# Kernel tuning notes

Measured on AMD Instinct MI355X. Metric: run time of the kernel, lower is better.

## Reference

```python
import jax, jax.numpy as jnp
import numpy as np

NUM_EMBEDDINGS = 1024
EMBEDDING_DIM = 64
COMMITMENT_COST = 0.25


def setup_inputs() -> dict:
    key = jax.random.key(0)
    k1, k2 = jax.random.split(key)
    inputs = jax.random.normal(k1, (64, 32, 32, EMBEDDING_DIM), dtype=jnp.float32)
    # torch init is uniform(-1/K, 1/K); scale accordingly
    weight = jax.random.uniform(
        k2, (NUM_EMBEDDINGS, EMBEDDING_DIM), dtype=jnp.float32,
        minval=-1.0 / NUM_EMBEDDINGS, maxval=1.0 / NUM_EMBEDDINGS)
    return {"inputs": inputs, "weight": weight}


def reference(inputs, weight):
    input_shape = inputs.shape
    flat = inputs.reshape(-1, EMBEDDING_DIM)               # [N, D]
    distances = (jnp.sum(flat ** 2, axis=1, keepdims=True)
                 + jnp.sum(weight ** 2, axis=1)
                 - 2.0 * flat @ weight.T)                   # [N, K]
    encoding_indices = jnp.argmin(distances, axis=1)        # [N]
    # gather codes (equivalent to one-hot @ weight, but as a direct gather)
    quantized = weight[encoding_indices].reshape(input_shape)

    e_latent_loss = jnp.mean((jax.lax.stop_gradient(quantized) - inputs) ** 2)
    q_latent_loss = jnp.mean((quantized - jax.lax.stop_gradient(inputs)) ** 2)
    loss = q_latent_loss + COMMITMENT_COST * e_latent_loss

    # straight-through estimator
    quantized_ste = inputs + jax.lax.stop_gradient(quantized - inputs)

    # perplexity (equivalent to mean over the one-hot encodings)
    n_tokens = flat.shape[0]
    counts = jax.ops.segment_sum(
        jnp.ones((n_tokens,), jnp.float32), encoding_indices,
        num_segments=NUM_EMBEDDINGS)
    avg_probs = counts / n_tokens
    perplexity = jnp.exp(-jnp.sum(avg_probs * jnp.log(avg_probs + 1e-10)))

    indices_for_transformer = encoding_indices.reshape(input_shape[0], -1)
    return (loss, quantized_ste, perplexity, indices_for_transformer)
```

## Files before the change

### kernel.cpp

```cpp
#include <hip/hip_runtime.h>
#include <cstdint>
#include <cstddef>

#define N_TOKENS 65536
#define DIM 64
#define K_CODES 1024
#define NTH 256
#define TPB 128
#define NCH 16

#define OFF_Q 1
#define OFF_PERP 4194305
#define OFF_IDX 4194306

#define MARGIN 1.5e-4f

#define WS_LOSS   0
#define WS_FCNT   8
#define WS_COUNTS 16
#define WS_WHI    4112
#define WS_WLO    135184
#define WS_S2     266256
#define WS_FLIST  270352

typedef __attribute__((ext_vector_type(8))) short  s16x8;
typedef __attribute__((ext_vector_type(4))) float  f32x4;

__device__ __forceinline__ float fmulr(float a, float b){ return __fmul_rn(a,b); }
__device__ __forceinline__ float faddr(float a, float b){ return __fadd_rn(a,b); }

__device__ __forceinline__ unsigned short f2bf(float f) {
    unsigned u = __float_as_uint(f);
    unsigned r = u + 0x7fffu + ((u >> 16) & 1u);
    return (unsigned short)(r >> 16);
}
__device__ __forceinline__ float bf2f(unsigned short h) {
    return __uint_as_float(((unsigned)h) << 16);
}

__device__ float sumsq64_np(const float* __restrict__ p) {
    float s[16];
    #pragma unroll
    for (int l = 0; l < 16; ++l) {
        float a0 = fmulr(p[l],      p[l]);
        float a1 = fmulr(p[l + 16], p[l + 16]);
        float a2 = fmulr(p[l + 32], p[l + 32]);
        float a3 = fmulr(p[l + 48], p[l + 48]);
        s[l] = faddr(faddr(a0, a1), faddr(a2, a3));
    }
    #pragma unroll
    for (int len = 8; len >= 1; len >>= 1)
        #pragma unroll
        for (int l = 0; l < len; ++l)
            s[l] = faddr(s[l], s[l + len]);
    return s[0];
}

__device__ __forceinline__ void async_copy16(const void* g, void* l) {
    __builtin_amdgcn_global_load_lds(
        (const __attribute__((address_space(1))) void*)g,
        (__attribute__((address_space(3))) void*)l, 16, 0, 0);
}

__global__ void vq_prep(const float* __restrict__ W, unsigned short* __restrict__ Whi,
                        unsigned short* __restrict__ Wlo, float* __restrict__ s2g,
                        int* __restrict__ counts, int* __restrict__ gfcount,
                        double* __restrict__ loss_acc) {
    int gid = blockIdx.x * NTH + threadIdx.x;
    for (int e = gid; e < K_CODES * DIM; e += 16384) {
        float x = W[e];
        unsigned short hi = f2bf(x);
        unsigned short lo = f2bf(__fsub_rn(x, bf2f(hi)));
        int j = e >> 6, k = e & 63;
        int pos = j * 64 + (((k >> 3) ^ (j & 7)) << 3) + (k & 7);
        Whi[pos] = hi; Wlo[pos] = lo;
    }
    if (gid < K_CODES) { s2g[gid] = sumsq64_np(W + gid * 64); counts[gid] = 0; }
    if (gid == 0) { *loss_acc = 0.0; *gfcount = 0; }
}

__global__ __launch_bounds__(NTH, 2)
void vq_main(const float* __restrict__ X, const float* __restrict__ W,
             const unsigned short* __restrict__ WhiG, const unsigned short* __restrict__ WloG,
             const float* __restrict__ s2g, float* __restrict__ out,
             double* __restrict__ loss_acc, int* __restrict__ counts,
             int* __restrict__ gfcount, unsigned short* __restrict__ gflist) {
    __shared__ __align__(16) unsigned short xs_hi[TPB * 64];
    __shared__ __align__(16) unsigned short xs_lo[TPB * 64];
    __shared__ __align__(16) unsigned short ws_hi[2][64 * 64];
    __shared__ __align__(16) unsigned short ws_lo[2][64 * 64];
    __shared__ __align__(16) float s2s[K_CODES];
    __shared__ int fidx[TPB];
    __shared__ int flist[TPB];
    __shared__ int fcount, gbaseS;
    __shared__ double lred[4];

    const int tid  = threadIdx.x;
    const int lane = tid & 63, wave = tid >> 6;
    const int quad = lane >> 4, lrow = lane & 15;
    const int t0   = blockIdx.x * TPB;

    if (tid == 0) fcount = 0;

    {
        const char* gh = (const char*)WhiG;
        const char* gl = (const char*)WloG;
        char* lh = (char*)&ws_hi[0][0] + wave * 1024;
        char* ll = (char*)&ws_lo[0][0] + wave * 1024;
        #pragma unroll
        for (int i = 0; i < 2; ++i) {
            async_copy16(gh + i * 4096 + tid * 16, lh + i * 4096);
            async_copy16(gl + i * 4096 + tid * 16, ll + i * 4096);
        }
    }
    *(f32x4*)&s2s[tid * 4] = *(const f32x4*)&s2g[tid * 4];
    #pragma unroll
    for (int i = 0; i < 4; ++i) {
        int g = tid + NTH * i;
        int t = g >> 3, kb = g & 7;
        const float* src = X + (size_t)(t0 + t) * DIM + kb * 8;
        float v[8];
        *(f32x4*)v       = *(const f32x4*)src;
        *(f32x4*)(v + 4) = *(const f32x4*)(src + 4);
        unsigned short h[8], l[8];
        #pragma unroll
        for (int k = 0; k < 8; ++k) {
            h[k] = f2bf(v[k]);
            l[k] = f2bf(__fsub_rn(v[k], bf2f(h[k])));
        }
        int base = t * 64 + ((kb ^ (t & 7)) << 3);
        *(s16x8*)&xs_hi[base] = *(s16x8*)h;
        *(s16x8*)&xs_lo[base] = *(s16x8*)l;
    }
    __syncthreads();

    s16x8 a_h0[2], a_h1[2], a_l0[2], a_l1[2];
    #pragma unroll
    for (int rt = 0; rt < 2; ++rt) {
        int tf = wave * 32 + rt * 16 + lrow;
        int sA = tf & 7;
        a_h0[rt] = *(const s16x8*)&xs_hi[tf * 64 + (((0 + quad) ^ sA) << 3)];
        a_h1[rt] = *(const s16x8*)&xs_hi[tf * 64 + (((4 + quad) ^ sA) << 3)];
        a_l0[rt] = *(const s16x8*)&xs_lo[tf * 64 + (((0 + quad) ^ sA) << 3)];
        a_l1[rt] = *(const s16x8*)&xs_lo[tf * 64 + (((4 + quad) ^ sA) << 3)];
    }

    float r1v[8], r2v[8]; int r1i[8];
    #pragma unroll
    for (int ri = 0; ri < 8; ++ri) { r1v[ri] = 3.4e38f; r2v[ri] = 3.4e38f; r1i[ri] = 0x7fffffff; }

    for (int ch = 0; ch < NCH; ++ch) {
        const int buf = ch & 1;
        if (ch < NCH - 1) {
            const char* gh = (const char*)WhiG + (ch + 1) * 8192;
            const char* gl = (const char*)WloG + (ch + 1) * 8192;
            char* lh = (char*)&ws_hi[buf ^ 1][0] + wave * 1024;
            char* ll = (char*)&ws_lo[buf ^ 1][0] + wave * 1024;
            #pragma unroll
            for (int i = 0; i < 2; ++i) {
                async_copy16(gh + i * 4096 + tid * 16, lh + i * 4096);
                async_copy16(gl + i * 4096 + tid * 16, ll + i * 4096);
            }
        }
        #pragma unroll
        for (int ct = 0; ct < 4; ++ct) {
            int lc = ct * 16 + lrow;
            int sB = lrow & 7;
            const unsigned short* bh = &ws_hi[buf][lc * 64];
            const unsigned short* bl = &ws_lo[buf][lc * 64];
            s16x8 b_h0 = *(const s16x8*)&bh[((0 + quad) ^ sB) << 3];
            s16x8 b_h1 = *(const s16x8*)&bh[((4 + quad) ^ sB) << 3];
            s16x8 b_l0 = *(const s16x8*)&bl[((0 + quad) ^ sB) << 3];
            s16x8 b_l1 = *(const s16x8*)&bl[((4 + quad) ^ sB) << 3];
            int jcode = ch * 64 + lc;
            float s2v = s2s[jcode];
            float ainit = fmulr(-0.5f, s2v);
            #pragma unroll
            for (int rt = 0; rt < 2; ++rt) {
                f32x4 acc = {ainit, ainit, ainit, ainit};
                acc = __builtin_amdgcn_mfma_f32_16x16x32_bf16(a_h0[rt], b_h0, acc, 0, 0, 0);
                acc = __builtin_amdgcn_mfma_f32_16x16x32_bf16(a_h1[rt], b_h1, acc, 0, 0, 0);
                acc = __builtin_amdgcn_mfma_f32_16x16x32_bf16(a_h0[rt], b_l0, acc, 0, 0, 0);
                acc = __builtin_amdgcn_mfma_f32_16x16x32_bf16(a_h1[rt], b_l1, acc, 0, 0, 0);
                acc = __builtin_amdgcn_mfma_f32_16x16x32_bf16(a_l0[rt], b_h0, acc, 0, 0, 0);
                acc = __builtin_amdgcn_mfma_f32_16x16x32_bf16(a_l1[rt], b_h1, acc, 0, 0, 0);
                #pragma unroll
                for (int r = 0; r < 4; ++r) {
                    float d = fmulr(-2.0f, acc[r]);
                    int ri = rt * 4 + r;
                    bool lt = d < r1v[ri];
                    float sec = lt ? r1v[ri] : d;
                    r2v[ri] = fminf(r2v[ri], sec);
                    r1v[ri] = lt ? d : r1v[ri];
                    r1i[ri] = lt ? jcode : r1i[ri];
                }
            }
        }
        __syncthreads();
    }

    #pragma unroll
    for (int m = 1; m <= 8; m <<= 1) {
        #pragma unroll
        for (int ri = 0; ri < 8; ++ri) {
            float o1v = __shfl_xor(r1v[ri], m, 64);
            int   o1i = __shfl_xor(r1i[ri], m, 64);
            float o2v = __shfl_xor(r2v[ri], m, 64);
            bool take = (o1v < r1v[ri]) || (o1v == r1v[ri] && o1i < r1i[ri]);
            float loser = take ? r1v[ri] : o1v;
            r2v[ri] = fminf(fminf(r2v[ri], o2v), loser);
            if (take) { r1v[ri] = o1v; r1i[ri] = o1i; }
        }
    }
    if (lrow == 0) {
        #pragma unroll
        for (int ri = 0; ri < 8; ++ri) {
            int rt = ri >> 2, r = ri & 3;
            int t = wave * 32 + rt * 16 + quad * 4 + r;
            bool fb = (r2v[ri] - r1v[ri]) < MARGIN;
            fidx[t] = fb ? (r1i[ri] | (int)0x80000000) : r1i[ri];
            if (fb) { int p = atomicAdd(&fcount, 1); flist[p] = t; }
        }
    }
    __syncthreads();

    double lsum = 0.0;
    #pragma unroll
    for (int i = 0; i < 8; ++i) {
        int e4 = tid + NTH * i;
        int t = e4 >> 4, d4 = (e4 & 15) * 4;
        int iv = fidx[t];
        if (iv >= 0) {
            f32x4 q = *(const f32x4*)&W[iv * 64 + d4];
            f32x4 x = *(const f32x4*)&X[(size_t)(t0 + t) * 64 + d4];
            *(f32x4*)&out[(size_t)OFF_Q + (size_t)(t0 + t) * 64 + d4] = q;
            #pragma unroll
            for (int c = 0; c < 4; ++c) {
                float df = __fsub_rn(q[c], x[c]);
                lsum += (double)fmulr(df, df);
            }
        }
    }
    #pragma unroll
    for (int off = 32; off >= 1; off >>= 1) lsum += __shfl_down(lsum, off, 64);
    if (lane == 0) lred[wave] = lsum;
    if (tid < TPB) {
        int iv = fidx[tid];
        if (iv >= 0) {
            atomicAdd(&counts[iv], 1);
            out[(size_t)OFF_IDX + t0 + tid] = (float)iv;
        }
    }
    if (tid == 0) gbaseS = atomicAdd(gfcount, fcount);
    __syncthreads();
    if (tid < fcount) gflist[gbaseS + tid] = (unsigned short)(t0 + flist[tid]);
    if (tid == 0) atomicAdd(loss_acc, lred[0] + lred[1] + lred[2] + lred[3]);
}

__global__ __launch_bounds__(NTH, 3)
void vq_fallback(const float* __restrict__ X, const float* __restrict__ W,
                 const float* __restrict__ s2g, const int* __restrict__ gfcount,
                 const unsigned short* __restrict__ gflist, float* __restrict__ out,
                 double* __restrict__ loss_acc, int* __restrict__ counts) {
    int count = *gfcount;
    int base = blockIdx.x * 64;
    if (base >= count) return;
    int nt = min(64, count - base);

    __shared__ __align__(16) float xsf[64 * 64];
    __shared__ __align__(16) float wsf[128 * 64];
    __shared__ float s1f[64];
    __shared__ int gidx[64];
    __shared__ double lredf[4];

    const int tid = threadIdx.x;
    const int lane = tid & 63, wave = tid >> 6;
    const int r = tid & 15, c = tid >> 4;

    #pragma unroll
    for (int i = 0; i < 4; ++i) {
        int idx = tid + NTH * i;
        int t = idx >> 4, kb = idx & 15;
        int tok = gflist[base + (t < nt ? t : 0)];
        f32x4 v = *(const f32x4*)(X + (size_t)tok * 64 + kb * 4);
        *(f32x4*)&xsf[t * 64 + ((kb ^ ((t >> 2) & 7)) << 2)] = v;
    }
    if (tid < nt) s1f[tid] = sumsq64_np(X + (size_t)gflist[base + tid] * 64);

    float runVal[4]; int runIdx[4];
    #pragma unroll
    for (int i = 0; i < 4; ++i) { runVal[i] = 3.4e38f; runIdx[i] = 0; }

    for (int ch = 0; ch < 8; ++ch) {
        __syncthreads();
        #pragma unroll
        for (int i = 0; i < 8; ++i) {
            int idx = tid + NTH * i;
            int jl = idx >> 4, kb = idx & 15;
            f32x4 v = *(const f32x4*)(W + (size_t)(ch * 128 + jl) * 64 + kb * 4);
            *(f32x4*)&wsf[jl * 64 + ((kb ^ ((jl >> 3) & 7)) << 2)] = v;
        }
        __syncthreads();

        float acc[4][8];
        #pragma unroll
        for (int i = 0; i < 4; ++i)
            #pragma unroll
            for (int m = 0; m < 8; ++m) acc[i][m] = 0.0f;

        #pragma unroll
        for (int kb = 0; kb < 16; ++kb) {
            f32x4 xv[4], wv[8];
            #pragma unroll
            for (int i = 0; i < 4; ++i)
                xv[i] = *(const f32x4*)&xsf[(4 * r + i) * 64 + ((kb ^ (r & 7)) << 2)];
            #pragma unroll
            for (int m = 0; m < 8; ++m)
                wv[m] = *(const f32x4*)&wsf[(8 * c + m) * 64 + ((kb ^ (c & 7)) << 2)];
            #pragma unroll
            for (int i = 0; i < 4; ++i)
                #pragma unroll
                for (int m = 0; m < 8; ++m) {
                    acc[i][m] = __builtin_fmaf(xv[i][0], wv[m][0], acc[i][m]);
                    acc[i][m] = __builtin_fmaf(xv[i][1], wv[m][1], acc[i][m]);
                    acc[i][m] = __builtin_fmaf(xv[i][2], wv[m][2], acc[i][m]);
                    acc[i][m] = __builtin_fmaf(xv[i][3], wv[m][3], acc[i][m]);
                }
        }
        #pragma unroll
        for (int i = 0; i < 4; ++i) {
            float s1v = s1f[4 * r + i];
            #pragma unroll
            for (int m = 0; m < 8; ++m) {
                int jl = 8 * c + m;
                float d = faddr(faddr(s1v, s2g[ch * 128 + jl]), fmulr(-2.0f, acc[i][m]));
                if (d < runVal[i]) { runVal[i] = d; runIdx[i] = ch * 128 + jl; }
            }
        }
    }

    __syncthreads();
    unsigned long long* red = (unsigned long long*)wsf;
    #pragma unroll
    for (int i = 0; i < 4; ++i) {
        unsigned long long pk =
            ((unsigned long long)__float_as_uint(runVal[i]) << 32) |
            (unsigned long long)(unsigned int)runIdx[i];
        red[(4 * r + i) * 16 + c] = pk;
    }
    __syncthreads();
    if (tid < 64) {
        unsigned long long best = red[tid * 16];
        #pragma unroll
        for (int cc = 1; cc < 16; ++cc) {
            unsigned long long v = red[tid * 16 + cc];
            best = (v < best) ? v : best;
        }
        int idx = (int)(best & 0xffffffffu);
        gidx[tid] = idx;
        if (tid < nt) {
            int tok = gflist[base + tid];
            out[(size_t)OFF_IDX + tok] = (float)idx;
            atomicAdd(&counts[idx], 1);
        }
    }
    __syncthreads();
    double lsum = 0.0;
    #pragma unroll
    for (int i = 0; i < 4; ++i) {
        int e4 = tid + NTH * i;
        int t = e4 >> 4, d4 = (e4 & 15) * 4;
        if (t < nt) {
            int tok = gflist[base + t];
            int idx = gidx[t];
            f32x4 q = *(const f32x4*)&W[idx * 64 + d4];
            f32x4 x = *(const f32x4*)&X[(size_t)tok * 64 + d4];
            *(f32x4*)&out[(size_t)OFF_Q + (size_t)tok * 64 + d4] = q;
            #pragma unroll
            for (int cc = 0; cc < 4; ++cc) {
                float df = __fsub_rn(q[cc], x[cc]);
                lsum += (double)fmulr(df, df);
            }
        }
    }
    #pragma unroll
    for (int off = 32; off >= 1; off >>= 1) lsum += __shfl_down(lsum, off, 64);
    if (lane == 0) lredf[wave] = lsum;
    __syncthreads();
    if (tid == 0) atomicAdd(loss_acc, lredf[0] + lredf[1] + lredf[2] + lredf[3]);
}

__global__ void vq_final(const int* __restrict__ counts,
                         const double* __restrict__ loss_acc,
                         float* __restrict__ out) {
    __shared__ double hred[4];
    int tid = threadIdx.x;
    double h = 0.0;
    for (int j = tid; j < K_CODES; j += 256) {
        double p = (double)counts[j] / 65536.0;
        h += p * log(p + 1e-10);
    }
    #pragma unroll
    for (int off = 32; off >= 1; off >>= 1) h += __shfl_down(h, off, 64);
    if ((tid & 63) == 0) hred[tid >> 6] = h;
    __syncthreads();
    if (tid == 0) {
        double H = hred[0] + hred[1] + hred[2] + hred[3];
        out[OFF_PERP] = (float)exp(-H);
        double ls = *loss_acc;
        float Lf = (float)(ls / 4194304.0);
        out[0] = faddr(Lf, fmulr(0.25f, Lf));
    }
}

extern "C" void kernel_launch(void* const* d_in, const int* in_sizes, int n_in,
                              void* d_out, int out_size, void* d_ws, size_t ws_size,
                              hipStream_t stream) {
    const float* X = (const float*)d_in[0];
    const float* W = (const float*)d_in[1];
    float* out = (float*)d_out;
    char* ws = (char*)d_ws;
    double* loss_acc = (double*)(ws + WS_LOSS);
    int* gfcount = (int*)(ws + WS_FCNT);
    int* counts = (int*)(ws + WS_COUNTS);
    unsigned short* Whi = (unsigned short*)(ws + WS_WHI);
    unsigned short* Wlo = (unsigned short*)(ws + WS_WLO);
    float* s2g = (float*)(ws + WS_S2);
    unsigned short* gflist = (unsigned short*)(ws + WS_FLIST);

    vq_prep<<<64, NTH, 0, stream>>>(W, Whi, Wlo, s2g, counts, gfcount, loss_acc);
    vq_main<<<N_TOKENS / TPB, NTH, 0, stream>>>(X, W, Whi, Wlo, s2g, out,
                                                loss_acc, counts, gfcount, gflist);
    vq_fallback<<<N_TOKENS / 64, NTH, 0, stream>>>(X, W, s2g, gfcount, gflist,
                                                   out, loss_acc, counts);
    vq_final<<<1, NTH, 0, stream>>>(counts, loss_acc, out);
}
```

Measured before the change: 171.4 us.

## Switch split-precision MFMA to scaled fp16, inline fallback and fuse final reduction

Replaces the bf16 hi/lo split with a scaled fp16 hi/lo split. fp16 keeps more mantissa bits, so the ambiguity margin can be tightened and fewer tokens need the exact fp32 fallback. Ambiguous tokens are now recomputed inside the main kernel, one wave per token, and the last block to finish (tracked with a ticket counter) computes perplexity and loss. This removes the separate fallback and final kernels. Tokens per block double to 256 with occupancy 1, which adds register pressure and reduces latency hiding. The in-block fallback reads W straight from global memory, serialising per wave.

```diff
diff --git a/kernel.cpp b/kernel.cpp
--- a/kernel.cpp
+++ b/kernel.cpp
@@ -6,36 +6,41 @@
 #define DIM 64
 #define K_CODES 1024
 #define NTH 256
-#define TPB 128
+#define TPB 256
 #define NCH 16
+#define NBLK (N_TOKENS / TPB)
 
 #define OFF_Q 1
 #define OFF_PERP 4194305
 #define OFF_IDX 4194306
 
-#define MARGIN 1.5e-4f
+#define MARGIN 2.5e-5f
+#define XSCALE 1024.0f
+#define WSCALE 65536.0f
+#define AINIT_SC -33554432.0f
+#define D_UNSC  -2.9802322387695312e-08f
 
 #define WS_LOSS   0
-#define WS_FCNT   8
+#define WS_TICKET 8
 #define WS_COUNTS 16
 #define WS_WHI    4112
 #define WS_WLO    135184
 #define WS_S2     266256
-#define WS_FLIST  270352
-
-typedef __attribute__((ext_vector_type(8))) short  s16x8;
-typedef __attribute__((ext_vector_type(4))) float  f32x4;
+
+typedef _Float16 f16x8 __attribute__((ext_vector_type(8)));
+typedef float    f32x4 __attribute__((ext_vector_type(4)));
 
 __device__ __forceinline__ float fmulr(float a, float b){ return __fmul_rn(a,b); }
 __device__ __forceinline__ float faddr(float a, float b){ return __fadd_rn(a,b); }
 
-__device__ __forceinline__ unsigned short f2bf(float f) {
+__device__ __forceinline__ unsigned keyf(float f) {
     unsigned u = __float_as_uint(f);
-    unsigned r = u + 0x7fffu + ((u >> 16) & 1u);
-    return (unsigned short)(r >> 16);
-}
-__device__ __forceinline__ float bf2f(unsigned short h) {
-    return __uint_as_float(((unsigned)h) << 16);
+    return u ^ ((u & 0x80000000u) ? 0xffffffffu : 0x80000000u);
+}
+
+__device__ __forceinline__ void split16(float v, _Float16& h, _Float16& l) {
+    h = (_Float16)v;
+    l = (_Float16)(v - (float)h);
 }
 
 __device__ float sumsq64_np(const float* __restrict__ p) {
@@ -62,37 +67,36 @@
         (__attribute__((address_space(3))) void*)l, 16, 0, 0);
 }
 
-__global__ void vq_prep(const float* __restrict__ W, unsigned short* __restrict__ Whi,
-                        unsigned short* __restrict__ Wlo, float* __restrict__ s2g,
-                        int* __restrict__ counts, int* __restrict__ gfcount,
+__global__ void vq_prep(const float* __restrict__ W, _Float16* __restrict__ Whi,
+                        _Float16* __restrict__ Wlo, float* __restrict__ s2g,
+                        int* __restrict__ counts, int* __restrict__ ticket,
                         double* __restrict__ loss_acc) {
     int gid = blockIdx.x * NTH + threadIdx.x;
     for (int e = gid; e < K_CODES * DIM; e += 16384) {
-        float x = W[e];
-        unsigned short hi = f2bf(x);
-        unsigned short lo = f2bf(__fsub_rn(x, bf2f(hi)));
+        float vs = W[e] * WSCALE;
+        _Float16 h, l; split16(vs, h, l);
         int j = e >> 6, k = e & 63;
         int pos = j * 64 + (((k >> 3) ^ (j & 7)) << 3) + (k & 7);
-        Whi[pos] = hi; Wlo[pos] = lo;
+        Whi[pos] = h; Wlo[pos] = l;
     }
     if (gid < K_CODES) { s2g[gid] = sumsq64_np(W + gid * 64); counts[gid] = 0; }
-    if (gid == 0) { *loss_acc = 0.0; *gfcount = 0; }
-}
-
-__global__ __launch_bounds__(NTH, 2)
+    if (gid == 0) { *loss_acc = 0.0; *ticket = 0; }
+}
+
+__global__ __launch_bounds__(NTH, 1)
 void vq_main(const float* __restrict__ X, const float* __restrict__ W,
-             const unsigned short* __restrict__ WhiG, const unsigned short* __restrict__ WloG,
+             const _Float16* __restrict__ WhiG, const _Float16* __restrict__ WloG,
              const float* __restrict__ s2g, float* __restrict__ out,
              double* __restrict__ loss_acc, int* __restrict__ counts,
-             int* __restrict__ gfcount, unsigned short* __restrict__ gflist) {
-    __shared__ __align__(16) unsigned short xs_hi[TPB * 64];
-    __shared__ __align__(16) unsigned short xs_lo[TPB * 64];
-    __shared__ __align__(16) unsigned short ws_hi[2][64 * 64];
-    __shared__ __align__(16) unsigned short ws_lo[2][64 * 64];
+             int* __restrict__ ticket) {
+    __shared__ __align__(16) _Float16 xs_hi[TPB * 64];
+    __shared__ __align__(16) _Float16 xs_lo[TPB * 64];
+    __shared__ __align__(16) _Float16 ws_hi[2][64 * 64];
+    __shared__ __align__(16) _Float16 ws_lo[2][64 * 64];
     __shared__ __align__(16) float s2s[K_CODES];
     __shared__ int fidx[TPB];
     __shared__ int flist[TPB];
-    __shared__ int fcount, gbaseS;
+    __shared__ int fcount, lastFlag;
     __shared__ double lred[4];
 
     const int tid  = threadIdx.x;
@@ -115,39 +119,36 @@
     }
     *(f32x4*)&s2s[tid * 4] = *(const f32x4*)&s2g[tid * 4];
     #pragma unroll
-    for (int i = 0; i < 4; ++i) {
+    for (int i = 0; i < 8; ++i) {
         int g = tid + NTH * i;
         int t = g >> 3, kb = g & 7;
         const float* src = X + (size_t)(t0 + t) * DIM + kb * 8;
         float v[8];
         *(f32x4*)v       = *(const f32x4*)src;
         *(f32x4*)(v + 4) = *(const f32x4*)(src + 4);
-        unsigned short h[8], l[8];
-        #pragma unroll
-        for (int k = 0; k < 8; ++k) {
-            h[k] = f2bf(v[k]);
-            l[k] = f2bf(__fsub_rn(v[k], bf2f(h[k])));
-        }
+        _Float16 h[8], l[8];
+        #pragma unroll
+        for (int k = 0; k < 8; ++k) split16(v[k] * XSCALE, h[k], l[k]);
         int base = t * 64 + ((kb ^ (t & 7)) << 3);
-        *(s16x8*)&xs_hi[base] = *(s16x8*)h;
-        *(s16x8*)&xs_lo[base] = *(s16x8*)l;
-    }
-    __syncthreads();
-
-    s16x8 a_h0[2], a_h1[2], a_l0[2], a_l1[2];
-    #pragma unroll
-    for (int rt = 0; rt < 2; ++rt) {
-        int tf = wave * 32 + rt * 16 + lrow;
+        *(f16x8*)&xs_hi[base] = *(f16x8*)h;
+        *(f16x8*)&xs_lo[base] = *(f16x8*)l;
+    }
+    __syncthreads();
+
+    f16x8 a_h0[4], a_h1[4], a_l0[4], a_l1[4];
+    #pragma unroll
+    for (int rt = 0; rt < 4; ++rt) {
+        int tf = wave * 64 + rt * 16 + lrow;
         int sA = tf & 7;
-        a_h0[rt] = *(const s16x8*)&xs_hi[tf * 64 + (((0 + quad) ^ sA) << 3)];
-        a_h1[rt] = *(const s16x8*)&xs_hi[tf * 64 + (((4 + quad) ^ sA) << 3)];
-        a_l0[rt] = *(const s16x8*)&xs_lo[tf * 64 + (((0 + quad) ^ sA) << 3)];
-        a_l1[rt] = *(const s16x8*)&xs_lo[tf * 64 + (((4 + quad) ^ sA) << 3)];
-    }
-
-    float r1v[8], r2v[8]; int r1i[8];
-    #pragma unroll
-    for (int ri = 0; ri < 8; ++ri) { r1v[ri] = 3.4e38f; r2v[ri] = 3.4e38f; r1i[ri] = 0x7fffffff; }
+        a_h0[rt] = *(const f16x8*)&xs_hi[tf * 64 + (((0 + quad) ^ sA) << 3)];
+        a_h1[rt] = *(const f16x8*)&xs_hi[tf * 64 + (((4 + quad) ^ sA) << 3)];
+        a_l0[rt] = *(const f16x8*)&xs_lo[tf * 64 + (((0 + quad) ^ sA) << 3)];
+        a_l1[rt] = *(const f16x8*)&xs_lo[tf * 64 + (((4 + quad) ^ sA) << 3)];
+    }
+
+    float r1v[16], r2v[16]; int r1i[16];
+    #pragma unroll
+    for (int ri = 0; ri < 16; ++ri) { r1v[ri] = 3.4e38f; r2v[ri] = 3.4e38f; r1i[ri] = 0x7fffffff; }
 
     for (int ch = 0; ch < NCH; ++ch) {
         const int buf = ch & 1;
@@ -166,27 +167,26 @@
         for (int ct = 0; ct < 4; ++ct) {
             int lc = ct * 16 + lrow;
             int sB = lrow & 7;
-            const unsigned short* bh = &ws_hi[buf][lc * 64];
-            const unsigned short* bl = &ws_lo[buf][lc * 64];
-            s16x8 b_h0 = *(const s16x8*)&bh[((0 + quad) ^ sB) << 3];
-            s16x8 b_h1 = *(const s16x8*)&bh[((4 + quad) ^ sB) << 3];
-            s16x8 b_l0 = *(const s16x8*)&bl[((0 + quad) ^ sB) << 3];
-            s16x8 b_l1 = *(const s16x8*)&bl[((4 + quad) ^ sB) << 3];
+            const _Float16* bh = &ws_hi[buf][lc * 64];
+            const _Float16* bl = &ws_lo[buf][lc * 64];
+            f16x8 b_h0 = *(const f16x8*)&bh[((0 + quad) ^ sB) << 3];
+            f16x8 b_h1 = *(const f16x8*)&bh[((4 + quad) ^ sB) << 3];
+            f16x8 b_l0 = *(const f16x8*)&bl[((0 + quad) ^ sB) << 3];
+            f16x8 b_l1 = *(const f16x8*)&bl[((4 + quad) ^ sB) << 3];
             int jcode = ch * 64 + lc;
-            float s2v = s2s[jcode];
-            float ainit = fmulr(-0.5f, s2v);
+            float ainit = fmulr(s2s[jcode], AINIT_SC);
             #pragma unroll
-            for (int rt = 0; rt < 2; ++rt) {
+            for (int rt = 0; rt < 4; ++rt) {
                 f32x4 acc = {ainit, ainit, ainit, ainit};
-                acc = __builtin_amdgcn_mfma_f32_16x16x32_bf16(a_h0[rt], b_h0, acc, 0, 0, 0);
-                acc = __builtin_amdgcn_mfma_f32_16x16x32_bf16(a_h1[rt], b_h1, acc, 0, 0, 0);
-                acc = __builtin_amdgcn_mfma_f32_16x16x32_bf16(a_h0[rt], b_l0, acc, 0, 0, 0);
-                acc = __builtin_amdgcn_mfma_f32_16x16x32_bf16(a_h1[rt], b_l1, acc, 0, 0, 0);
-                acc = __builtin_amdgcn_mfma_f32_16x16x32_bf16(a_l0[rt], b_h0, acc, 0, 0, 0);
-                acc = __builtin_amdgcn_mfma_f32_16x16x32_bf16(a_l1[rt], b_h1, acc, 0, 0, 0);
+                acc = __builtin_amdgcn_mfma_f32_16x16x32_f16(a_h0[rt], b_h0, acc, 0, 0, 0);
+                acc = __builtin_amdgcn_mfma_f32_16x16x32_f16(a_h1[rt], b_h1, acc, 0, 0, 0);
+                acc = __builtin_amdgcn_mfma_f32_16x16x32_f16(a_h0[rt], b_l0, acc, 0, 0, 0);
+                acc = __builtin_amdgcn_mfma_f32_16x16x32_f16(a_h1[rt], b_l1, acc, 0, 0, 0);
+                acc = __builtin_amdgcn_mfma_f32_16x16x32_f16(a_l0[rt], b_h0, acc, 0, 0, 0);
+                acc = __builtin_amdgcn_mfma_f32_16x16x32_f16(a_l1[rt], b_h1, acc, 0, 0, 0);
                 #pragma unroll
                 for (int r = 0; r < 4; ++r) {
-                    float d = fmulr(-2.0f, acc[r]);
+                    float d = fmulr(acc[r], D_UNSC);
                     int ri = rt * 4 + r;
                     bool lt = d < r1v[ri];
                     float sec = lt ? r1v[ri] : d;
@@ -202,7 +202,7 @@
     #pragma unroll
     for (int m = 1; m <= 8; m <<= 1) {
         #pragma unroll
-        for (int ri = 0; ri < 8; ++ri) {
+        for (int ri = 0; ri < 16; ++ri) {
             float o1v = __shfl_xor(r1v[ri], m, 64);
             int   o1i = __shfl_xor(r1i[ri], m, 64);
             float o2v = __shfl_xor(r2v[ri], m, 64);
@@ -214,9 +214,9 @@
     }
     if (lrow == 0) {
         #pragma unroll
-        for (int ri = 0; ri < 8; ++ri) {
+        for (int ri = 0; ri < 16; ++ri) {
             int rt = ri >> 2, r = ri & 3;
-            int t = wave * 32 + rt * 16 + quad * 4 + r;
+            int t = wave * 64 + rt * 16 + quad * 4 + r;
             bool fb = (r2v[ri] - r1v[ri]) < MARGIN;
             fidx[t] = fb ? (r1i[ri] | (int)0x80000000) : r1i[ri];
             if (fb) { int p = atomicAdd(&fcount, 1); flist[p] = t; }
@@ -226,7 +226,7 @@
 
     double lsum = 0.0;
     #pragma unroll
-    for (int i = 0; i < 8; ++i) {
+    for (int i = 0; i < 16; ++i) {
         int e4 = tid + NTH * i;
         int t = e4 >> 4, d4 = (e4 & 15) * 4;
         int iv = fidx[t];
@@ -251,165 +251,80 @@
             out[(size_t)OFF_IDX + t0 + tid] = (float)iv;
         }
     }
-    if (tid == 0) gbaseS = atomicAdd(gfcount, fcount);
-    __syncthreads();
-    if (tid < fcount) gflist[gbaseS + tid] = (unsigned short)(t0 + flist[tid]);
+    __syncthreads();
     if (tid == 0) atomicAdd(loss_acc, lred[0] + lred[1] + lred[2] + lred[3]);
-}
-
-__global__ __launch_bounds__(NTH, 3)
-void vq_fallback(const float* __restrict__ X, const float* __restrict__ W,
-                 const float* __restrict__ s2g, const int* __restrict__ gfcount,
-                 const unsigned short* __restrict__ gflist, float* __restrict__ out,
-                 double* __restrict__ loss_acc, int* __restrict__ counts) {
-    int count = *gfcount;
-    int base = blockIdx.x * 64;
-    if (base >= count) return;
-    int nt = min(64, count - base);
-
-    __shared__ __align__(16) float xsf[64 * 64];
-    __shared__ __align__(16) float wsf[128 * 64];
-    __shared__ float s1f[64];
-    __shared__ int gidx[64];
-    __shared__ double lredf[4];
-
-    const int tid = threadIdx.x;
-    const int lane = tid & 63, wave = tid >> 6;
-    const int r = tid & 15, c = tid >> 4;
-
-    #pragma unroll
-    for (int i = 0; i < 4; ++i) {
-        int idx = tid + NTH * i;
-        int t = idx >> 4, kb = idx & 15;
-        int tok = gflist[base + (t < nt ? t : 0)];
-        f32x4 v = *(const f32x4*)(X + (size_t)tok * 64 + kb * 4);
-        *(f32x4*)&xsf[t * 64 + ((kb ^ ((t >> 2) & 7)) << 2)] = v;
-    }
-    if (tid < nt) s1f[tid] = sumsq64_np(X + (size_t)gflist[base + tid] * 64);
-
-    float runVal[4]; int runIdx[4];
-    #pragma unroll
-    for (int i = 0; i < 4; ++i) { runVal[i] = 3.4e38f; runIdx[i] = 0; }
-
-    for (int ch = 0; ch < 8; ++ch) {
+
+    for (int fi = wave; fi < fcount; fi += 4) {
+        int t = flist[fi];
+        int gtok = t0 + t;
+        float s1v = sumsq64_np(X + (size_t)gtok * 64);
+        f32x4 xr[16];
+        #pragma unroll
+        for (int kb = 0; kb < 16; ++kb)
+            xr[kb] = *(const f32x4*)(X + (size_t)gtok * 64 + kb * 4);
+        unsigned long long best = ~0ULL;
+        #pragma unroll 1
+        for (int c16 = 0; c16 < 16; ++c16) {
+            int code = lane * 16 + c16;
+            const float* wr = W + code * 64;
+            float acc = 0.0f;
+            #pragma unroll
+            for (int kb = 0; kb < 16; ++kb) {
+                f32x4 wv = *(const f32x4*)(wr + kb * 4);
+                acc = __builtin_fmaf(xr[kb][0], wv[0], acc);
+                acc = __builtin_fmaf(xr[kb][1], wv[1], acc);
+                acc = __builtin_fmaf(xr[kb][2], wv[2], acc);
+                acc = __builtin_fmaf(xr[kb][3], wv[3], acc);
+            }
+            float d = faddr(faddr(s1v, s2s[code]), fmulr(-2.0f, acc));
+            unsigned long long pk = ((unsigned long long)keyf(d) << 32) | (unsigned)code;
+            best = pk < best ? pk : best;
+        }
+        #pragma unroll
+        for (int m = 32; m >= 1; m >>= 1) {
+            unsigned long long o = __shfl_xor(best, m, 64);
+            best = o < best ? o : best;
+        }
+        int idx = (int)(best & 0xffffffffu);
+        float q = W[idx * 64 + lane];
+        float x = X[(size_t)gtok * 64 + lane];
+        out[(size_t)OFF_Q + (size_t)gtok * 64 + lane] = q;
+        float df = __fsub_rn(q, x);
+        double ls = (double)fmulr(df, df);
+        #pragma unroll
+        for (int m = 32; m >= 1; m >>= 1) ls += __shfl_xor(ls, m, 64);
+        if (lane == 0) {
+            out[(size_t)OFF_IDX + gtok] = (float)idx;
+            atomicAdd(&counts[idx], 1);
+            atomicAdd(loss_acc, ls);
+        }
+    }
+
+    __syncthreads();
+    if (tid == 0) {
+        __threadfence();
+        int old = atomicAdd(ticket, 1);
+        lastFlag = (old == NBLK - 1) ? 1 : 0;
+    }
+    __syncthreads();
+    if (lastFlag) {
+        double h = 0.0;
+        for (int j = tid; j < K_CODES; j += NTH) {
+            int c = atomicAdd(&counts[j], 0);
+            double p = (double)c / 65536.0;
+            h += p * log(p + 1e-10);
+        }
+        #pragma unroll
+        for (int off = 32; off >= 1; off >>= 1) h += __shfl_down(h, off, 64);
+        if (lane == 0) lred[wave] = h;
         __syncthreads();
-        #pragma unroll
-        for (int i = 0; i < 8; ++i) {
-            int idx = tid + NTH * i;
-            int jl = idx >> 4, kb = idx & 15;
-            f32x4 v = *(const f32x4*)(W + (size_t)(ch * 128 + jl) * 64 + kb * 4);
-            *(f32x4*)&wsf[jl * 64 + ((kb ^ ((jl >> 3) & 7)) << 2)] = v;
-        }
-        __syncthreads();
-
-        float acc[4][8];
-        #pragma unroll
-        for (int i = 0; i < 4; ++i)
-            #pragma unroll
-            for (int m = 0; m < 8; ++m) acc[i][m] = 0.0f;
-
-        #pragma unroll
-        for (int kb = 0; kb < 16; ++kb) {
-            f32x4 xv[4], wv[8];
-            #pragma unroll
-            for (int i = 0; i < 4; ++i)
-                xv[i] = *(const f32x4*)&xsf[(4 * r + i) * 64 + ((kb ^ (r & 7)) << 2)];
-            #pragma unroll
-            for (int m = 0; m < 8; ++m)
-                wv[m] = *(const f32x4*)&wsf[(8 * c + m) * 64 + ((kb ^ (c & 7)) << 2)];
-            #pragma unroll
-            for (int i = 0; i < 4; ++i)
-                #pragma unroll
-                for (int m = 0; m < 8; ++m) {
-                    acc[i][m] = __builtin_fmaf(xv[i][0], wv[m][0], acc[i][m]);
-                    acc[i][m] = __builtin_fmaf(xv[i][1], wv[m][1], acc[i][m]);
-                    acc[i][m] = __builtin_fmaf(xv[i][2], wv[m][2], acc[i][m]);
-                    acc[i][m] = __builtin_fmaf(xv[i][3], wv[m][3], acc[i][m]);
-                }
-        }
-        #pragma unroll
-        for (int i = 0; i < 4; ++i) {
-            float s1v = s1f[4 * r + i];
-            #pragma unroll
-            for (int m = 0; m < 8; ++m) {
-                int jl = 8 * c + m;
-                float d = faddr(faddr(s1v, s2g[ch * 128 + jl]), fmulr(-2.0f, acc[i][m]));
-                if (d < runVal[i]) { runVal[i] = d; runIdx[i] = ch * 128 + jl; }
-            }
-        }
-    }
-
-    __syncthreads();
-    unsigned long long* red = (unsigned long long*)wsf;
-    #pragma unroll
-    for (int i = 0; i < 4; ++i) {
-        unsigned long long pk =
-            ((unsigned long long)__float_as_uint(runVal[i]) << 32) |
-            (unsigned long long)(unsigned int)runIdx[i];
-        red[(4 * r + i) * 16 + c] = pk;
-    }
-    __syncthreads();
-    if (tid < 64) {
-        unsigned long long best = red[tid * 16];
-        #pragma unroll
-        for (int cc = 1; cc < 16; ++cc) {
-            unsigned long long v = red[tid * 16 + cc];
-            best = (v < best) ? v : best;
-        }
-        int idx = (int)(best & 0xffffffffu);
-        gidx[tid] = idx;
-        if (tid < nt) {
-            int tok = gflist[base + tid];
-            out[(size_t)OFF_IDX + tok] = (float)idx;
-            atomicAdd(&counts[idx], 1);
-        }
-    }
-    __syncthreads();
-    double lsum = 0.0;
-    #pragma unroll
-    for (int i = 0; i < 4; ++i) {
-        int e4 = tid + NTH * i;
-        int t = e4 >> 4, d4 = (e4 & 15) * 4;
-        if (t < nt) {
-            int tok = gflist[base + t];
-            int idx = gidx[t];
-            f32x4 q = *(const f32x4*)&W[idx * 64 + d4];
-            f32x4 x = *(const f32x4*)&X[(size_t)tok * 64 + d4];
-            *(f32x4*)&out[(size_t)OFF_Q + (size_t)tok * 64 + d4] = q;
-            #pragma unroll
-            for (int cc = 0; cc < 4; ++cc) {
-                float df = __fsub_rn(q[cc], x[cc]);
-                lsum += (double)fmulr(df, df);
-            }
-        }
-    }
-    #pragma unroll
-    for (int off = 32; off >= 1; off >>= 1) lsum += __shfl_down(lsum, off, 64);
-    if (lane == 0) lredf[wave] = lsum;
-    __syncthreads();
-    if (tid == 0) atomicAdd(loss_acc, lredf[0] + lredf[1] + lredf[2] + lredf[3]);
-}
-
-__global__ void vq_final(const int* __restrict__ counts,
-                         const double* __restrict__ loss_acc,
-                         float* __restrict__ out) {
-    __shared__ double hred[4];
-    int tid = threadIdx.x;
-    double h = 0.0;
-    for (int j = tid; j < K_CODES; j += 256) {
-        double p = (double)counts[j] / 65536.0;
-        h += p * log(p + 1e-10);
-    }
-    #pragma unroll
-    for (int off = 32; off >= 1; off >>= 1) h += __shfl_down(h, off, 64);
-    if ((tid & 63) == 0) hred[tid >> 6] = h;
-    __syncthreads();
-    if (tid == 0) {
-        double H = hred[0] + hred[1] + hred[2] + hred[3];
-        out[OFF_PERP] = (float)exp(-H);
-        double ls = *loss_acc;
-        float Lf = (float)(ls / 4194304.0);
-        out[0] = faddr(Lf, fmulr(0.25f, Lf));
+        if (tid == 0) {
+            double H = lred[0] + lred[1] + lred[2] + lred[3];
+            out[OFF_PERP] = (float)exp(-H);
+            double ls = atomicAdd(loss_acc, 0.0);
+            float Lf = (float)(ls / 4194304.0);
+            out[0] = faddr(Lf, fmulr(0.25f, Lf));
+        }
     }
 }
 
@@ -421,17 +336,13 @@
     float* out = (float*)d_out;
     char* ws = (char*)d_ws;
     double* loss_acc = (double*)(ws + WS_LOSS);
-    int* gfcount = (int*)(ws + WS_FCNT);
+    int* ticket = (int*)(ws + WS_TICKET);
     int* counts = (int*)(ws + WS_COUNTS);
-    unsigned short* Whi = (unsigned short*)(ws + WS_WHI);
-    unsigned short* Wlo = (unsigned short*)(ws + WS_WLO);
+    _Float16* Whi = (_Float16*)(ws + WS_WHI);
+    _Float16* Wlo = (_Float16*)(ws + WS_WLO);
     float* s2g = (float*)(ws + WS_S2);
-    unsigned short* gflist = (unsigned short*)(ws + WS_FLIST);
-
-    vq_prep<<<64, NTH, 0, stream>>>(W, Whi, Wlo, s2g, counts, gfcount, loss_acc);
-    vq_main<<<N_TOKENS / TPB, NTH, 0, stream>>>(X, W, Whi, Wlo, s2g, out,
-                                                loss_acc, counts, gfcount, gflist);
-    vq_fallback<<<N_TOKENS / 64, NTH, 0, stream>>>(X, W, s2g, gfcount, gflist,
-                                                   out, loss_acc, counts);
-    vq_final<<<1, NTH, 0, stream>>>(counts, loss_acc, out);
-}
+
+    vq_prep<<<64, NTH, 0, stream>>>(W, Whi, Wlo, s2g, counts, ticket, loss_acc);
+    vq_main<<<NBLK, NTH, 0, stream>>>(X, W, Whi, Wlo, s2g, out,
+                                      loss_acc, counts, ticket);
+}
```

Result: slower. 204.8 us (+19.5%).
